# Kernel tuning notes

Measured on AMD Instinct MI355X. Metric: run time of the kernel, lower is better.

The kernel has to match this reference:

```python
import jax, jax.numpy as jnp
import numpy as np

TEMPERATURE = 22.627417  # ~sqrt(512)


def setup_inputs() -> dict:
    key = jax.random.key(0)
    ks = jax.random.split(key, 7)
    B, NP, NQ, D = 4, 256, 256, 512
    return {
        "q": jax.random.normal(ks[0], (B, NP, D), jnp.float32),
        "k": jax.random.normal(ks[1], (B, NP, D), jnp.float32),
        "v": jax.random.normal(ks[2], (B, NP, D), jnp.float32),
        "query": jax.random.normal(ks[3], (B, NQ, D), jnp.float32),
        "query_q": jax.random.normal(ks[4], (B, NQ, D), jnp.float32),
        "query_k": jax.random.normal(ks[5], (B, NP, D), jnp.float32),
        "query_v": jax.random.normal(ks[6], (B, NQ, D), jnp.float32),
    }


def reference(q, k, v, query, query_q, query_k, query_v):
    # Self-attention block over prototypes: [B, NP, NP]
    scores = jnp.einsum("bpd,bqd->bpq", q, k) / TEMPERATURE
    log_attn = jax.nn.log_softmax(scores, axis=2)
    attn = jax.nn.softmax(scores, axis=2)
    # NOTE: torch.bmm(attn, v) in the original is dead code (overwritten), so it is skipped.

    # Query-gated attention: [B, NQ, NP]
    q_scores = jnp.einsum("bnd,bpd->bnp", query_q, query_k) / TEMPERATURE
    query_attn = jax.nn.softmax(q_scores, axis=2)

    # Gated broadcast combine: [B, NQ, NP, D]
    # query_attn * v_rep + query_attn * query_v == query_attn * (v + query_v)
    gate = query_attn[:, :, :, None]            # [B, NQ, NP, 1]
    combined = v[:, None, :, :] + query_v[:, :, None, :]  # [B, NQ, NP, D]
    output = gate * combined
    return (output, attn, log_attn)
```

## Files before the change

kernel.cpp:

```cpp
#include <hip/hip_runtime.h>
#include <math.h>

#define BB   4
#define NP   256
#define NQ   256
#define DD   512
#define DD4  (DD / 4)

typedef float f32x4 __attribute__((ext_vector_type(4)));

static constexpr float kScale = 1.0f / 22.627417f;

__global__ __launch_bounds__(256) void fused_qgsa_kernel(
    const float* __restrict__ q,
    const float* __restrict__ k,
    const f32x4* __restrict__ v4,
    const float* __restrict__ qq,
    const float* __restrict__ qk,
    const f32x4* __restrict__ qv4,
    f32x4* __restrict__ out4,
    float* __restrict__ attn_out,
    float* __restrict__ logattn_out)
{
    __shared__ __align__(16) float smem[4 * 256];
    __shared__ float red[8];
    const int t = threadIdx.x;

    if (blockIdx.x < (unsigned)(BB * NQ)) {
        const int bn = blockIdx.x;
        const int b  = bn >> 8;
        const int n  = bn & (NQ - 1);
        const int w  = t >> 6;
        const int l  = t & 63;

        float val;
        {
            const f32x4* krow = (const f32x4*)(qk + ((size_t)b * NP + t) * DD);
            const float* qrow = qq + ((size_t)b * NQ + n) * DD;
            float acc = 0.f;
            #pragma unroll 8
            for (int d4 = 0; d4 < DD4; ++d4) {
                const f32x4 kv = krow[d4];
                const float* qr = qrow + d4 * 4;
                acc += qr[0] * kv.x + qr[1] * kv.y + qr[2] * kv.z + qr[3] * kv.w;
            }
            val = acc * kScale;
        }

        float m = val;
        #pragma unroll
        for (int off = 32; off >= 1; off >>= 1) m = fmaxf(m, __shfl_xor(m, off, 64));
        if (l == 0) red[w] = m;
        __syncthreads();
        m = fmaxf(fmaxf(red[0], red[1]), fmaxf(red[2], red[3]));

        const float e = expf(val - m);
        float s = e;
        #pragma unroll
        for (int off = 32; off >= 1; off >>= 1) s += __shfl_xor(s, off, 64);
        if (l == 0) red[4 + w] = s;
        __syncthreads();
        s = (red[4] + red[5]) + (red[6] + red[7]);

        smem[t] = e / s;
        __syncthreads();

        const int d4 = t & (DD4 - 1);
        const int po = t >> 7;
        const f32x4 qvr = qv4[((size_t)b * NQ + n) * DD4 + d4];
        const f32x4* vcol = v4 + (size_t)b * NP * DD4 + d4;
        f32x4* ocol = out4 + ((size_t)b * NQ + n) * ((size_t)NP * DD4) + d4;

        #pragma unroll 4
        for (int p = po; p < NP; p += 2) {
            const float gpn = smem[p];
            const f32x4 vv  = vcol[(size_t)p * DD4];
            const f32x4 o   = (vv + qvr) * gpn;
            __builtin_nontemporal_store(o, ocol + (size_t)p * DD4);
        }
    } else {
        const int idx = blockIdx.x - BB * NQ;
        const int b   = idx >> 6;
        const int p0  = (idx & 63) * 4;

        const f32x4* krow = (const f32x4*)(k + ((size_t)b * NP + t) * DD);
        const float* qb   = q + ((size_t)b * NP + p0) * DD;

        float acc[4] = {0.f, 0.f, 0.f, 0.f};
        #pragma unroll 8
        for (int d4 = 0; d4 < DD4; ++d4) {
            const f32x4 kv = krow[d4];
            #pragma unroll
            for (int r = 0; r < 4; ++r) {
                const float* qr = qb + r * DD + d4 * 4;
                acc[r] += qr[0] * kv.x + qr[1] * kv.y + qr[2] * kv.z + qr[3] * kv.w;
            }
        }

        float (*ss)[256] = (float (*)[256])smem;
        #pragma unroll
        for (int r = 0; r < 4; ++r) ss[r][t] = acc[r] * kScale;
        __syncthreads();

        const int r = t >> 6;
        const int g = t & 63;
        const f32x4 sv = ((const f32x4*)ss[r])[g];

        float m = fmaxf(fmaxf(sv.x, sv.y), fmaxf(sv.z, sv.w));
        #pragma unroll
        for (int off = 32; off >= 1; off >>= 1) m = fmaxf(m, __shfl_xor(m, off, 64));

        f32x4 ev;
        ev.x = expf(sv.x - m); ev.y = expf(sv.y - m);
        ev.z = expf(sv.z - m); ev.w = expf(sv.w - m);
        float s = (ev.x + ev.y) + (ev.z + ev.w);
        #pragma unroll
        for (int off = 32; off >= 1; off >>= 1) s += __shfl_xor(s, off, 64);

        const float inv = 1.0f / s;
        const float lse = logf(s);

        const size_t base = ((size_t)b * NP + (p0 + r)) * 256;
        ((f32x4*)(attn_out + base))[g] = ev * inv;
        f32x4 lg;
        lg.x = (sv.x - m) - lse; lg.y = (sv.y - m) - lse;
        lg.z = (sv.z - m) - lse; lg.w = (sv.w - m) - lse;
        ((f32x4*)(logattn_out + base))[g] = lg;
    }
}

extern "C" void kernel_launch(void* const* d_in, const int* in_sizes, int n_in,
                              void* d_out, int out_size, void* d_ws, size_t ws_size,
                              hipStream_t stream) {
    const float* q  = (const float*)d_in[0];
    const float* k  = (const float*)d_in[1];
    const float* v  = (const float*)d_in[2];
    const float* qq = (const float*)d_in[4];
    const float* qk = (const float*)d_in[5];
    const float* qv = (const float*)d_in[6];

    float* out = (float*)d_out;
    const size_t out_elems = (size_t)BB * NQ * NP * DD;
    float* attn_out    = out + out_elems;
    float* logattn_out = attn_out + (size_t)BB * NP * 256;

    fused_qgsa_kernel<<<BB * NQ + 256, 256, 0, stream>>>(
        q, k, (const f32x4*)v, qq, qk, (const f32x4*)qv,
        (f32x4*)out, attn_out, logattn_out);
}
```

Before: 131.9 us.

## Process two query rows per block to share K and V loads

New measurement: 137.5 us. +4.2%, slower.

```diff
diff --git a/kernel.cpp b/kernel.cpp
--- a/kernel.cpp
+++ b/kernel.cpp
@@ -11,7 +11,7 @@
 
 static constexpr float kScale = 1.0f / 22.627417f;
 
-__global__ __launch_bounds__(256) void fused_qgsa_kernel(
+__global__ __launch_bounds__(256) void fused_qgsa2_kernel(
     const float* __restrict__ q,
     const float* __restrict__ k,
     const f32x4* __restrict__ v4,
@@ -23,63 +23,74 @@
     float* __restrict__ logattn_out)
 {
     __shared__ __align__(16) float smem[4 * 256];
-    __shared__ float red[8];
     const int t = threadIdx.x;
 
-    if (blockIdx.x < (unsigned)(BB * NQ)) {
-        const int bn = blockIdx.x;
-        const int b  = bn >> 8;
-        const int n  = bn & (NQ - 1);
-        const int w  = t >> 6;
-        const int l  = t & 63;
+    if (blockIdx.x < 512u) {
+        const int b  = blockIdx.x >> 7;
+        const int n0 = (blockIdx.x & 127) * 2;
 
-        float val;
         {
             const f32x4* krow = (const f32x4*)(qk + ((size_t)b * NP + t) * DD);
-            const float* qrow = qq + ((size_t)b * NQ + n) * DD;
-            float acc = 0.f;
+            const float* qb   = qq + ((size_t)b * NQ + n0) * DD;
+            float acc0 = 0.f, acc1 = 0.f;
             #pragma unroll 8
             for (int d4 = 0; d4 < DD4; ++d4) {
                 const f32x4 kv = krow[d4];
-                const float* qr = qrow + d4 * 4;
-                acc += qr[0] * kv.x + qr[1] * kv.y + qr[2] * kv.z + qr[3] * kv.w;
+                const float* q0 = qb + d4 * 4;
+                const float* q1 = qb + DD + d4 * 4;
+                acc0 += q0[0] * kv.x + q0[1] * kv.y + q0[2] * kv.z + q0[3] * kv.w;
+                acc1 += q1[0] * kv.x + q1[1] * kv.y + q1[2] * kv.z + q1[3] * kv.w;
             }
-            val = acc * kScale;
+            smem[t]       = acc0 * kScale;
+            smem[256 + t] = acc1 * kScale;
         }
+        __syncthreads();
 
-        float m = val;
-        #pragma unroll
-        for (int off = 32; off >= 1; off >>= 1) m = fmaxf(m, __shfl_xor(m, off, 64));
-        if (l == 0) red[w] = m;
-        __syncthreads();
-        m = fmaxf(fmaxf(red[0], red[1]), fmaxf(red[2], red[3]));
+        {
+            const int r = (t >> 6) & 1;
+            const int g = t & 63;
+            const f32x4 sv = ((const f32x4*)(smem + r * 256))[g];
 
-        const float e = expf(val - m);
-        float s = e;
-        #pragma unroll
-        for (int off = 32; off >= 1; off >>= 1) s += __shfl_xor(s, off, 64);
-        if (l == 0) red[4 + w] = s;
-        __syncthreads();
-        s = (red[4] + red[5]) + (red[6] + red[7]);
+            float m = fmaxf(fmaxf(sv.x, sv.y), fmaxf(sv.z, sv.w));
+            #pragma unroll
+            for (int off = 32; off >= 1; off >>= 1)
+                m = fmaxf(m, __shfl_xor(m, off, 64));
 
-        smem[t] = e / s;
+            f32x4 ev;
+            ev.x = expf(sv.x - m); ev.y = expf(sv.y - m);
+            ev.z = expf(sv.z - m); ev.w = expf(sv.w - m);
+            float s = (ev.x + ev.y) + (ev.z + ev.w);
+            #pragma unroll
+            for (int off = 32; off >= 1; off >>= 1) s += __shfl_xor(s, off, 64);
+
+            const float inv = 1.0f / s;
+            float* gtf = smem + 512;
+            gtf[(4 * g + 0) * 2 + r] = ev.x * inv;
+            gtf[(4 * g + 1) * 2 + r] = ev.y * inv;
+            gtf[(4 * g + 2) * 2 + r] = ev.z * inv;
+            gtf[(4 * g + 3) * 2 + r] = ev.w * inv;
+        }
         __syncthreads();
 
         const int d4 = t & (DD4 - 1);
         const int po = t >> 7;
-        const f32x4 qvr = qv4[((size_t)b * NQ + n) * DD4 + d4];
+        const f32x4 qvr0 = qv4[((size_t)b * NQ + n0) * DD4 + d4];
+        const f32x4 qvr1 = qv4[((size_t)b * NQ + n0 + 1) * DD4 + d4];
         const f32x4* vcol = v4 + (size_t)b * NP * DD4 + d4;
-        f32x4* ocol = out4 + ((size_t)b * NQ + n) * ((size_t)NP * DD4) + d4;
+        f32x4* ocol = out4 + ((size_t)b * NQ + n0) * ((size_t)NP * DD4) + d4;
+        const float2* gt2 = (const float2*)(smem + 512);
 
         #pragma unroll 4
         for (int p = po; p < NP; p += 2) {
-            const float gpn = smem[p];
-            const f32x4 vv  = vcol[(size_t)p * DD4];
-            const f32x4 o   = (vv + qvr) * gpn;
-            __builtin_nontemporal_store(o, ocol + (size_t)p * DD4);
+            const f32x4 vv = vcol[(size_t)p * DD4];
+            const float2 g2 = gt2[p];
+            __builtin_nontemporal_store((vv + qvr0) * g2.x,
+                                        ocol + (size_t)p * DD4);
+            __builtin_nontemporal_store((vv + qvr1) * g2.y,
+                                        ocol + (size_t)(NP * DD4) + (size_t)p * DD4);
         }
     } else {
-        const int idx = blockIdx.x - BB * NQ;
+        const int idx = blockIdx.x - 512;
         const int b   = idx >> 6;
         const int p0  = (idx & 63) * 4;
 
@@ -108,7 +119,8 @@
 
         float m = fmaxf(fmaxf(sv.x, sv.y), fmaxf(sv.z, sv.w));
         #pragma unroll
-        for (int off = 32; off >= 1; off >>= 1) m = fmaxf(m, __shfl_xor(m, off, 64));
+        for (int off = 32; off >= 1; off >>= 1)
+            m = fmaxf(m, __shfl_xor(m, off, 64));
 
         f32x4 ev;
         ev.x = expf(sv.x - m); ev.y = expf(sv.y - m);
@@ -144,7 +156,7 @@
     float* attn_out    = out + out_elems;
     float* logattn_out = attn_out + (size_t)BB * NP * 256;
 
-    fused_qgsa_kernel<<<BB * NQ + 256, 256, 0, stream>>>(
+    fused_qgsa2_kernel<<<768, 256, 0, stream>>>(
         q, k, (const f32x4*)v, qq, qk, (const f32x4*)qv,
         (f32x4*)out, attn_out, logattn_out);
 }
```
